# Kernel tuning notes

Measured on AMD Instinct MI355X. Metric: run time of the kernel, lower is better.

## Reference

```python
import jax, jax.numpy as jnp
import numpy as np

BN_EPS = 1e-5


def setup_inputs() -> dict:
    key = jax.random.key(0)
    ks = jax.random.split(key, 6)
    B, C, N = 8, 256, 2048
    C4 = C // 4
    return {
        "x": jax.random.normal(ks[0], (B, C, N), dtype=jnp.float32),
        "wq": jax.random.normal(ks[1], (C4, C), dtype=jnp.float32) * (1.0 / np.sqrt(C)),
        "wv": jax.random.normal(ks[2], (C, C), dtype=jnp.float32) * (1.0 / np.sqrt(C)),
        "bv": jax.random.normal(ks[3], (C,), dtype=jnp.float32) * 0.02,
        "wt": jax.random.normal(ks[4], (C, C), dtype=jnp.float32) * (1.0 / np.sqrt(C)),
        "bt": jax.random.normal(ks[5], (C,), dtype=jnp.float32) * 0.02,
        "gamma": jnp.ones((C,), dtype=jnp.float32),
        "beta": jnp.zeros((C,), dtype=jnp.float32),
    }


def reference(x, wq, wv, bv, wt, bt, gamma, beta):
    # x: [B, C, N]. Conv1d(kernel=1) == per-point matmul.
    # q_conv and k_conv share the same weight in the original, so q == k.
    q = jnp.einsum('oc,bcn->bon', wq, x)            # [B, C/4, N]
    # ||q_i - q_j||_2 via the Gram identity (same math as norm of the diff tensor)
    sq = jnp.sum(q * q, axis=1)                     # [B, N]
    gram = jnp.einsum('bci,bcj->bij', q, q)         # [B, N, N]
    d2 = sq[:, :, None] - 2.0 * gram + sq[:, None, :]
    l2 = jnp.sqrt(jnp.maximum(d2, 0.0))             # [B, N, N]
    attn = jax.nn.softmax(-l2, axis=-1)             # rows = queries i
    v = jnp.einsum('oc,bcn->bon', wv, x) + bv[None, :, None]   # [B, C, N]
    # einsum('bij,bkj->bik') then permute(0,2,1) == contract j directly to [B, C, N]
    x_r = jnp.einsum('bij,bcj->bci', attn, v)       # [B, C, N]
    t = jnp.einsum('oc,bcn->bon', wt, x_r) + bt[None, :, None]
    # BatchNorm1d in training mode: batch stats over (B, N), biased variance
    mean = jnp.mean(t, axis=(0, 2), keepdims=True)
    var = jnp.mean((t - mean) ** 2, axis=(0, 2), keepdims=True)
    bn = gamma[None, :, None] * (t - mean) * jax.lax.rsqrt(var + BN_EPS) + beta[None, :, None]
    return x + jnp.maximum(bn, 0.0)
```

## Files before the change

### kernel.cpp

```cpp
#include <hip/hip_runtime.h>
#include <math.h>

#define BDIM 8
#define CDIM 256
#define C4DIM 64
#define NDIM 2048
#define LOG2E_SQ 2.0813689810056077f
#define NEG_2LOG2E_SQ -4.1627379620112154f

typedef short bf16x8 __attribute__((ext_vector_type(8)));
typedef float f32x4 __attribute__((ext_vector_type(4)));

__device__ inline unsigned cvt_pk(float lo, float hi) {
  unsigned r;
  asm("v_cvt_pk_bf16_f32 %0, %1, %2" : "=v"(r) : "v"(lo), "v"(hi));
  return r;
}
__device__ inline float bflo(unsigned u) {
  u <<= 16; float f; __builtin_memcpy(&f, &u, 4); return f;
}
__device__ inline float bfhi(unsigned u) {
  u &= 0xffff0000u; float f; __builtin_memcpy(&f, &u, 4); return f;
}

__global__ __launch_bounds__(256) void castw_kernel(const float* __restrict__ wq,
                                                    const float* __restrict__ wv,
                                                    const float* __restrict__ wt,
                                                    short* __restrict__ wqb,
                                                    short* __restrict__ wvb,
                                                    short* __restrict__ wtb) {
  const int idx = (blockIdx.x * 256 + threadIdx.x) * 4;
  const float* src; short* dst; int off;
  if (idx < 16384)       { src = wq; dst = wqb; off = idx; }
  else if (idx < 81920)  { src = wv; dst = wvb; off = idx - 16384; }
  else                   { src = wt; dst = wtb; off = idx - 81920; }
  float4 v = *(const float4*)&src[off];
  uint2 u = make_uint2(cvt_pk(v.x, v.y), cvt_pk(v.z, v.w));
  *(uint2*)&dst[off] = u;
}

__global__ __launch_bounds__(256) void castT_kernel(const float* __restrict__ x,
                                                    short* __restrict__ xT) {
  __shared__ float tile[64][65];
  const int b = blockIdx.z, c0 = blockIdx.y * 64, n0 = blockIdx.x * 64;
  const int t = threadIdx.x;
  const int cl = t >> 2, ng = (t & 3) * 16;
#pragma unroll
  for (int kk = 0; kk < 4; ++kk) {
    float4 v = *(const float4*)&x[((size_t)(b * CDIM + c0 + cl)) * NDIM + n0 + ng + kk * 4];
    tile[cl][ng + kk * 4 + 0] = v.x; tile[cl][ng + kk * 4 + 1] = v.y;
    tile[cl][ng + kk * 4 + 2] = v.z; tile[cl][ng + kk * 4 + 3] = v.w;
  }
  __syncthreads();
  const int nl = t >> 2, cg = (t & 3) * 16;
  unsigned u[8];
#pragma unroll
  for (int e = 0; e < 8; ++e)
    u[e] = cvt_pk(tile[cg + 2 * e][nl], tile[cg + 2 * e + 1][nl]);
  short* dst = &xT[((size_t)b * NDIM + n0 + nl) * CDIM + c0 + cg];
  *(uint4*)&dst[0] = make_uint4(u[0], u[1], u[2], u[3]);
  *(uint4*)&dst[8] = make_uint4(u[4], u[5], u[6], u[7]);
}

__global__ __launch_bounds__(256) void qgemm_kernel(const short* __restrict__ wqb,
                                                    const short* __restrict__ xT,
                                                    short* __restrict__ qT,
                                                    float* __restrict__ sq2) {
  const int b = blockIdx.y, n0 = blockIdx.x * 64;
  const int t = threadIdx.x, w = t >> 6, l = t & 63, il = l & 15, g = l >> 4;
  const int nw = n0 + w * 16;
  f32x4 acc[4] = {};
#pragma unroll
  for (int ks = 0; ks < 8; ++ks) {
    const int k0 = ks * 32;
    bf16x8 bx = *(const bf16x8*)&xT[((size_t)b * NDIM + nw + il) * CDIM + k0 + g * 8];
#pragma unroll
    for (int ot = 0; ot < 4; ++ot) {
      bf16x8 aw = *(const bf16x8*)&wqb[(size_t)(ot * 16 + il) * CDIM + k0 + g * 8];
      acc[ot] = __builtin_amdgcn_mfma_f32_16x16x32_bf16(aw, bx, acc[ot], 0, 0, 0);
    }
  }
  float sqs = 0.f;
#pragma unroll
  for (int ot = 0; ot < 4; ++ot) {
    unsigned u0 = cvt_pk(acc[ot][0], acc[ot][1]);
    unsigned u1 = cvt_pk(acc[ot][2], acc[ot][3]);
    *(uint2*)&qT[((size_t)b * NDIM + nw + il) * C4DIM + ot * 16 + g * 4] = make_uint2(u0, u1);
    float f0 = bflo(u0), f1 = bfhi(u0), f2 = bflo(u1), f3 = bfhi(u1);
    sqs += f0 * f0 + f1 * f1 + f2 * f2 + f3 * f3;
  }
  sqs += __shfl_xor(sqs, 16, 64);
  sqs += __shfl_xor(sqs, 32, 64);
  if (l < 16) sq2[(size_t)b * NDIM + nw + l] = sqs * LOG2E_SQ;
}

template<bool F32OUT>
__global__ __launch_bounds__(256) void vt_gemm(const short* __restrict__ Wb,
                                               const short* __restrict__ Xt,
                                               const float* __restrict__ bias,
                                               void* __restrict__ OUTP,
                                               float* __restrict__ bnsum,
                                               float* __restrict__ bnss) {
  const int b = blockIdx.z, n0 = blockIdx.x * 128, c0 = blockIdx.y * 128;
  const int t = threadIdx.x, w = t >> 6, l = t & 63, il = l & 15, g = l >> 4;
  const int wn = w & 1, wc = w >> 1;
  const size_t arow = (size_t)b * NDIM + n0 + wn * 64;
  const int ccol = c0 + wc * 64;
  f32x4 acc[4][4] = {};
#pragma unroll
  for (int ks = 0; ks < 8; ++ks) {
    const int k0 = ks * 32;
    bf16x8 af[4], bf[4];
#pragma unroll
    for (int nt = 0; nt < 4; ++nt)
      af[nt] = *(const bf16x8*)&Xt[(arow + nt * 16 + il) * CDIM + k0 + g * 8];
#pragma unroll
    for (int ct = 0; ct < 4; ++ct)
      bf[ct] = *(const bf16x8*)&Wb[(size_t)(ccol + ct * 16 + il) * CDIM + k0 + g * 8];
#pragma unroll
    for (int nt = 0; nt < 4; ++nt)
#pragma unroll
      for (int ct = 0; ct < 4; ++ct)
        acc[nt][ct] = __builtin_amdgcn_mfma_f32_16x16x32_bf16(af[nt], bf[ct], acc[nt][ct], 0, 0, 0);
  }
#pragma unroll
  for (int ct = 0; ct < 4; ++ct) {
    const int c = ccol + ct * 16 + il;
    const float bs = bias[c];
    float s = 0.f, ss = 0.f;
#pragma unroll
    for (int nt = 0; nt < 4; ++nt) {
      const int n = n0 + wn * 64 + nt * 16 + g * 4;
      float y0 = acc[nt][ct][0] + bs, y1 = acc[nt][ct][1] + bs;
      float y2 = acc[nt][ct][2] + bs, y3 = acc[nt][ct][3] + bs;
      if (F32OUT) {
        *(float4*)&((float*)OUTP)[((size_t)(b * CDIM + c)) * NDIM + n] =
            make_float4(y0, y1, y2, y3);
        s += y0 + y1 + y2 + y3;
        ss += y0 * y0 + y1 * y1 + y2 * y2 + y3 * y3;
      } else {
        *(uint2*)&((short*)OUTP)[((size_t)(b * CDIM + c)) * NDIM + n] =
            make_uint2(cvt_pk(y0, y1), cvt_pk(y2, y3));
      }
    }
    if (F32OUT) {
      s += __shfl_xor(s, 16, 64);   s += __shfl_xor(s, 32, 64);
      ss += __shfl_xor(ss, 16, 64); ss += __shfl_xor(ss, 32, 64);
      if (l < 16) { atomicAdd(&bnsum[c], s); atomicAdd(&bnss[c], ss); }
    }
  }
}

__global__ __launch_bounds__(512) void attn_mfma(const short* __restrict__ qT,
                                                 const short* __restrict__ Vb16,
                                                 const float* __restrict__ sq2,
                                                 short* __restrict__ xrT) {
  __shared__ __align__(16) short vj[2][256 * 32];
  __shared__ __align__(16) short qj[2][32 * 64];
  __shared__ __align__(16) short wlds[4][16][40];
  __shared__ float sums[8][16];

  const int b  = blockIdx.y;
  const int i0 = blockIdx.x * 64;
  const int t  = threadIdx.x;
  const int w  = t >> 6, l = t & 63;
  const int il = l & 15, g = l >> 4;
  const int isub = w & 3, chalf = w >> 2;

  const short* qTb = qT + (size_t)b * NDIM * C4DIM;
  const short* Vbb = Vb16 + (size_t)b * CDIM * NDIM;
  const float* sqb = sq2 + (size_t)b * NDIM;

  const int iglob = i0 + isub * 16 + il;
  const bf16x8 bq0 = *(const bf16x8*)&qTb[(size_t)iglob * C4DIM + g * 8];
  const bf16x8 bq1 = *(const bf16x8*)&qTb[(size_t)iglob * C4DIM + 32 + g * 8];
  const float sqi = sqb[iglob];

  const int vc0 = t >> 2, vs0 = t & 3;
  const int vc1 = 128 + (t >> 2);
  const int vd0 = vc0 * 32 + ((vs0 ^ ((vc0 >> 1) & 3)) << 3);
  const int vd1 = vc1 * 32 + ((vs0 ^ ((vc1 >> 1) & 3)) << 3);
  const int qrow = t >> 3, qslot = t & 7;
  const int qd = qrow * 64 + ((qslot ^ (qrow & 7)) << 3);

  f32x4 acc[8];
#pragma unroll
  for (int k = 0; k < 8; ++k) acc[k] = {0.f, 0.f, 0.f, 0.f};
  float sumw = 0.f;

  f32x4 sqc;
  {
    bf16x8 vr0 = *(const bf16x8*)&Vbb[(size_t)vc0 * NDIM + vs0 * 8];
    bf16x8 vr1 = *(const bf16x8*)&Vbb[(size_t)vc1 * NDIM + vs0 * 8];
    *(bf16x8*)&vj[0][vd0] = vr0;
    *(bf16x8*)&vj[0][vd1] = vr1;
    if (w < 4) {
      bf16x8 qr = *(const bf16x8*)&qTb[(size_t)qrow * C4DIM + qslot * 8];
      *(bf16x8*)&qj[0][qd] = qr;
    }
    sqc = *(const f32x4*)&sqb[chalf * 16 + g * 4];
  }
  __syncthreads();

  const int NT = NDIM / 32;
  for (int jt = 0; jt < NT; ++jt) {
    const int p = jt & 1;
    const short* vbuf = &vj[p][0];
    const short* qbuf = &qj[p][0];
    short* vbufN = &vj[p ^ 1][0];
    short* qbufN = &qj[p ^ 1][0];
    const bool has_next = (jt + 1 < NT);
    const int j0n = jt * 32 + 32;

    bf16x8 vr0 = {}, vr1 = {}, qr = {};
    f32x4 sqn = {};
    if (has_next) {
      vr0 = *(const bf16x8*)&Vbb[(size_t)vc0 * NDIM + j0n + vs0 * 8];
      vr1 = *(const bf16x8*)&Vbb[(size_t)vc1 * NDIM + j0n + vs0 * 8];
      if (w < 4) qr = *(const bf16x8*)&qTb[(size_t)(j0n + qrow) * C4DIM + qslot * 8];
      sqn = *(const f32x4*)&sqb[j0n + chalf * 16 + g * 4];
    }

    {
      const int row = chalf * 16 + il;
      bf16x8 aJ0 = *(const bf16x8*)&qbuf[row * 64 + ((g ^ (il & 7)) << 3)];
      bf16x8 aJ1 = *(const bf16x8*)&qbuf[row * 64 + (((4 + g) ^ (il & 7)) << 3)];
      f32x4 s = {0.f, 0.f, 0.f, 0.f};
      s = __builtin_amdgcn_mfma_f32_16x16x32_bf16(aJ0, bq0, s, 0, 0, 0);
      s = __builtin_amdgcn_mfma_f32_16x16x32_bf16(aJ1, bq1, s, 0, 0, 0);
      float wv[4];
#pragma unroll
      for (int r = 0; r < 4; ++r) {
        float e = fmaxf(fmaf(NEG_2LOG2E_SQ, s[r], sqi + sqc[r]), 0.f);
        wv[r] = __builtin_amdgcn_exp2f(-__builtin_amdgcn_sqrtf(e));
        sumw += wv[r];
      }
      *(uint2*)&wlds[isub][il][chalf * 16 + g * 4] =
          make_uint2(cvt_pk(wv[0], wv[1]), cvt_pk(wv[2], wv[3]));
    }
    __syncthreads();

    const bf16x8 bw = *(const bf16x8*)&wlds[isub][il][g * 8];
#pragma unroll
    for (int ctl = 0; ctl < 8; ++ctl) {
      const int c = (chalf * 8 + ctl) * 16 + il;
      bf16x8 aV = *(const bf16x8*)&vbuf[c * 32 + ((g ^ ((il >> 1) & 3)) << 3)];
      acc[ctl] = __builtin_amdgcn_mfma_f32_16x16x32_bf16(aV, bw, acc[ctl], 0, 0, 0);
    }

    if (has_next) {
      *(bf16x8*)&vbufN[vd0] = vr0;
      *(bf16x8*)&vbufN[vd1] = vr1;
      if (w < 4) *(bf16x8*)&qbufN[qd] = qr;
      sqc = sqn;
    }
    __syncthreads();
  }

  sumw += __shfl_xor(sumw, 16, 64);
  sumw += __shfl_xor(sumw, 32, 64);
  if (l < 16) sums[w][l] = sumw;
  __syncthreads();
  const float inv = 1.f / (sums[w][il] + sums[w ^ 4][il]);
#pragma unroll
  for (int ctl = 0; ctl < 8; ++ctl) {
    float y0 = acc[ctl][0] * inv, y1 = acc[ctl][1] * inv;
    float y2 = acc[ctl][2] * inv, y3 = acc[ctl][3] * inv;
    *(uint2*)&xrT[((size_t)b * NDIM + iglob) * CDIM + (chalf * 8 + ctl) * 16 + g * 4] =
        make_uint2(cvt_pk(y0, y1), cvt_pk(y2, y3));
  }
}

__global__ __launch_bounds__(256) void bn_small(const float* __restrict__ bnsum,
                                                const float* __restrict__ bnss,
                                                const float* __restrict__ gamma,
                                                const float* __restrict__ beta,
                                                float* __restrict__ scale,
                                                float* __restrict__ shift) {
  const int c = threadIdx.x;
  const float cnt = (float)(BDIM * NDIM);
  const float mean = bnsum[c] / cnt;
  const float var = fmaxf(bnss[c] / cnt - mean * mean, 0.f);
  const float sc = gamma[c] * rsqrtf(var + 1e-5f);
  scale[c] = sc;
  shift[c] = beta[c] - mean * sc;
}

__global__ __launch_bounds__(256) void final_kernel(const float* __restrict__ x,
                                                    const float* __restrict__ scale,
                                                    const float* __restrict__ shift,
                                                    float* __restrict__ out) {
  const size_t idx = ((size_t)blockIdx.x * 256 + threadIdx.x) << 2;
  const int c = (int)((idx >> 11) & 255);
  float4 xv = *(const float4*)&x[idx];
  float4 tv = *(const float4*)&out[idx];
  const float sc = scale[c], sh = shift[c];
  float4 r;
  r.x = xv.x + fmaxf(tv.x * sc + sh, 0.f);
  r.y = xv.y + fmaxf(tv.y * sc + sh, 0.f);
  r.z = xv.z + fmaxf(tv.z * sc + sh, 0.f);
  r.w = xv.w + fmaxf(tv.w * sc + sh, 0.f);
  *(float4*)&out[idx] = r;
}

extern "C" void kernel_launch(void* const* d_in, const int* in_sizes, int n_in,
                              void* d_out, int out_size, void* d_ws, size_t ws_size,
                              hipStream_t stream) {
  const float* x     = (const float*)d_in[0];
  const float* wq    = (const float*)d_in[1];
  const float* wv    = (const float*)d_in[2];
  const float* bv    = (const float*)d_in[3];
  const float* wt    = (const float*)d_in[4];
  const float* bt    = (const float*)d_in[5];
  const float* gamma = (const float*)d_in[6];
  const float* beta  = (const float*)d_in[7];
  float* out = (float*)d_out;
  char* ws = (char*)d_ws;

  short* xbT   = (short*)(ws);
  short* wqb   = (short*)(ws + ((size_t)9  << 20));
  short* wvb   = (short*)(ws + ((size_t)9  << 20) + (256 << 10));
  short* wtb   = (short*)(ws + ((size_t)9  << 20) + (512 << 10));
  short* qT    = (short*)(ws + ((size_t)10 << 20));
  float* sq2   = (float*)(ws + ((size_t)12 << 20));
  short* vbf   = (short*)(ws + ((size_t)13 << 20));
  short* xrT   = (short*)(ws + ((size_t)22 << 20));
  float* bnsum = (float*)(ws + ((size_t)31 << 20));
  float* bnss  = bnsum + 256;
  float* scale = bnsum + 512;
  float* shift = bnsum + 768;

  castw_kernel<<<dim3(144), 256, 0, stream>>>(wq, wv, wt, wqb, wvb, wtb);
  castT_kernel<<<dim3(NDIM / 64, CDIM / 64, BDIM), 256, 0, stream>>>(x, xbT);
  qgemm_kernel<<<dim3(NDIM / 64, BDIM), 256, 0, stream>>>(wqb, xbT, qT, sq2);
  vt_gemm<false><<<dim3(NDIM / 128, CDIM / 128, BDIM), 256, 0, stream>>>(
      wvb, xbT, bv, vbf, nullptr, nullptr);
  attn_mfma<<<dim3(NDIM / 64, BDIM), 512, 0, stream>>>(qT, vbf, sq2, xrT);
  hipMemsetAsync((void*)bnsum, 0, 2048, stream);
  vt_gemm<true><<<dim3(NDIM / 128, CDIM / 128, BDIM), 256, 0, stream>>>(
      wtb, xrT, bt, out, bnsum, bnss);
  bn_small<<<dim3(1), 256, 0, stream>>>(bnsum, bnss, gamma, beta, scale, shift);
  final_kernel<<<dim3((BDIM * CDIM * NDIM) / (256 * 4)), 256, 0, stream>>>(x, scale, shift, out);
}
```

Measured before the change: 116.5 us.

## Merge launches, split attention over channel halves, store BN input as bf16

Combines the weight cast, input transpose-cast and BN-accumulator zeroing into one prep kernel. It also merges the q and v GEMMs into one launch and folds the BN scale/shift computation into the final kernel, cutting the launch count from nine to five. The attention kernel now uses 256-thread blocks, each handling one channel half with a swizzled block order. This removes one barrier per tile and the cross-wave sum exchange, but each block recomputes the distance weights for both halves. The pre-BN activations are written as bf16 instead of fp32, reducing traffic at the cost of precision in the batch-norm input.

```diff
diff --git a/kernel.cpp b/kernel.cpp
--- a/kernel.cpp
+++ b/kernel.cpp
@@ -23,86 +23,57 @@
   u &= 0xffff0000u; float f; __builtin_memcpy(&f, &u, 4); return f;
 }
 
-__global__ __launch_bounds__(256) void castw_kernel(const float* __restrict__ wq,
-                                                    const float* __restrict__ wv,
-                                                    const float* __restrict__ wt,
-                                                    short* __restrict__ wqb,
-                                                    short* __restrict__ wvb,
-                                                    short* __restrict__ wtb) {
-  const int idx = (blockIdx.x * 256 + threadIdx.x) * 4;
-  const float* src; short* dst; int off;
-  if (idx < 16384)       { src = wq; dst = wqb; off = idx; }
-  else if (idx < 81920)  { src = wv; dst = wvb; off = idx - 16384; }
-  else                   { src = wt; dst = wtb; off = idx - 81920; }
-  float4 v = *(const float4*)&src[off];
-  uint2 u = make_uint2(cvt_pk(v.x, v.y), cvt_pk(v.z, v.w));
-  *(uint2*)&dst[off] = u;
-}
-
-__global__ __launch_bounds__(256) void castT_kernel(const float* __restrict__ x,
-                                                    short* __restrict__ xT) {
+__global__ __launch_bounds__(256) void prep_kernel(const float* __restrict__ x,
+                                                   const float* __restrict__ wq,
+                                                   const float* __restrict__ wv,
+                                                   const float* __restrict__ wt,
+                                                   short* __restrict__ xT,
+                                                   short* __restrict__ wqb,
+                                                   short* __restrict__ wvb,
+                                                   short* __restrict__ wtb,
+                                                   float* __restrict__ bnsum) {
   __shared__ float tile[64][65];
-  const int b = blockIdx.z, c0 = blockIdx.y * 64, n0 = blockIdx.x * 64;
-  const int t = threadIdx.x;
-  const int cl = t >> 2, ng = (t & 3) * 16;
-#pragma unroll
-  for (int kk = 0; kk < 4; ++kk) {
-    float4 v = *(const float4*)&x[((size_t)(b * CDIM + c0 + cl)) * NDIM + n0 + ng + kk * 4];
-    tile[cl][ng + kk * 4 + 0] = v.x; tile[cl][ng + kk * 4 + 1] = v.y;
-    tile[cl][ng + kk * 4 + 2] = v.z; tile[cl][ng + kk * 4 + 3] = v.w;
-  }
-  __syncthreads();
-  const int nl = t >> 2, cg = (t & 3) * 16;
-  unsigned u[8];
-#pragma unroll
-  for (int e = 0; e < 8; ++e)
-    u[e] = cvt_pk(tile[cg + 2 * e][nl], tile[cg + 2 * e + 1][nl]);
-  short* dst = &xT[((size_t)b * NDIM + n0 + nl) * CDIM + c0 + cg];
-  *(uint4*)&dst[0] = make_uint4(u[0], u[1], u[2], u[3]);
-  *(uint4*)&dst[8] = make_uint4(u[4], u[5], u[6], u[7]);
-}
-
-__global__ __launch_bounds__(256) void qgemm_kernel(const short* __restrict__ wqb,
-                                                    const short* __restrict__ xT,
-                                                    short* __restrict__ qT,
-                                                    float* __restrict__ sq2) {
-  const int b = blockIdx.y, n0 = blockIdx.x * 64;
-  const int t = threadIdx.x, w = t >> 6, l = t & 63, il = l & 15, g = l >> 4;
-  const int nw = n0 + w * 16;
-  f32x4 acc[4] = {};
-#pragma unroll
-  for (int ks = 0; ks < 8; ++ks) {
-    const int k0 = ks * 32;
-    bf16x8 bx = *(const bf16x8*)&xT[((size_t)b * NDIM + nw + il) * CDIM + k0 + g * 8];
-#pragma unroll
-    for (int ot = 0; ot < 4; ++ot) {
-      bf16x8 aw = *(const bf16x8*)&wqb[(size_t)(ot * 16 + il) * CDIM + k0 + g * 8];
-      acc[ot] = __builtin_amdgcn_mfma_f32_16x16x32_bf16(aw, bx, acc[ot], 0, 0, 0);
-    }
-  }
-  float sqs = 0.f;
-#pragma unroll
-  for (int ot = 0; ot < 4; ++ot) {
-    unsigned u0 = cvt_pk(acc[ot][0], acc[ot][1]);
-    unsigned u1 = cvt_pk(acc[ot][2], acc[ot][3]);
-    *(uint2*)&qT[((size_t)b * NDIM + nw + il) * C4DIM + ot * 16 + g * 4] = make_uint2(u0, u1);
-    float f0 = bflo(u0), f1 = bfhi(u0), f2 = bflo(u1), f3 = bfhi(u1);
-    sqs += f0 * f0 + f1 * f1 + f2 * f2 + f3 * f3;
-  }
-  sqs += __shfl_xor(sqs, 16, 64);
-  sqs += __shfl_xor(sqs, 32, 64);
-  if (l < 16) sq2[(size_t)b * NDIM + nw + l] = sqs * LOG2E_SQ;
-}
-
-template<bool F32OUT>
-__global__ __launch_bounds__(256) void vt_gemm(const short* __restrict__ Wb,
-                                               const short* __restrict__ Xt,
-                                               const float* __restrict__ bias,
-                                               void* __restrict__ OUTP,
-                                               float* __restrict__ bnsum,
-                                               float* __restrict__ bnss) {
-  const int b = blockIdx.z, n0 = blockIdx.x * 128, c0 = blockIdx.y * 128;
-  const int t = threadIdx.x, w = t >> 6, l = t & 63, il = l & 15, g = l >> 4;
+  const int fb = blockIdx.x, t = threadIdx.x;
+  if (fb < 1024) {
+    const int b = fb >> 7, c0 = ((fb >> 5) & 3) * 64, n0 = (fb & 31) * 64;
+    const int cl = t >> 2, ng = (t & 3) * 16;
+#pragma unroll
+    for (int kk = 0; kk < 4; ++kk) {
+      float4 v = *(const float4*)&x[((size_t)(b * CDIM + c0 + cl)) * NDIM + n0 + ng + kk * 4];
+      tile[cl][ng + kk * 4 + 0] = v.x; tile[cl][ng + kk * 4 + 1] = v.y;
+      tile[cl][ng + kk * 4 + 2] = v.z; tile[cl][ng + kk * 4 + 3] = v.w;
+    }
+    __syncthreads();
+    const int nl = t >> 2, cg = (t & 3) * 16;
+    unsigned u[8];
+#pragma unroll
+    for (int e = 0; e < 8; ++e)
+      u[e] = cvt_pk(tile[cg + 2 * e][nl], tile[cg + 2 * e + 1][nl]);
+    short* dst = &xT[((size_t)b * NDIM + n0 + nl) * CDIM + c0 + cg];
+    *(uint4*)&dst[0] = make_uint4(u[0], u[1], u[2], u[3]);
+    *(uint4*)&dst[8] = make_uint4(u[4], u[5], u[6], u[7]);
+  } else if (fb < 1168) {
+    const int idx = ((fb - 1024) * 256 + t) * 4;
+    const float* src; short* dst; int off;
+    if (idx < 16384)      { src = wq; dst = wqb; off = idx; }
+    else if (idx < 81920) { src = wv; dst = wvb; off = idx - 16384; }
+    else                  { src = wt; dst = wtb; off = idx - 81920; }
+    float4 v = *(const float4*)&src[off];
+    *(uint2*)&dst[off] = make_uint2(cvt_pk(v.x, v.y), cvt_pk(v.z, v.w));
+  } else {
+    bnsum[t] = 0.f; bnsum[256 + t] = 0.f;
+  }
+}
+
+template<bool STATS>
+__device__ __forceinline__ void gemm128(const short* __restrict__ Wb,
+                                        const short* __restrict__ Xt,
+                                        const float* __restrict__ bias,
+                                        short* __restrict__ OUT,
+                                        float* __restrict__ bnsum,
+                                        float* __restrict__ bnss,
+                                        int b, int n0, int c0, int t) {
+  const int w = t >> 6, l = t & 63, il = l & 15, g = l >> 4;
   const int wn = w & 1, wc = w >> 1;
   const size_t arow = (size_t)b * NDIM + n0 + wn * 64;
   const int ccol = c0 + wc * 64;
@@ -110,18 +81,18 @@
 #pragma unroll
   for (int ks = 0; ks < 8; ++ks) {
     const int k0 = ks * 32;
-    bf16x8 af[4], bf[4];
+    bf16x8 af[4], bfr[4];
 #pragma unroll
     for (int nt = 0; nt < 4; ++nt)
       af[nt] = *(const bf16x8*)&Xt[(arow + nt * 16 + il) * CDIM + k0 + g * 8];
 #pragma unroll
     for (int ct = 0; ct < 4; ++ct)
-      bf[ct] = *(const bf16x8*)&Wb[(size_t)(ccol + ct * 16 + il) * CDIM + k0 + g * 8];
+      bfr[ct] = *(const bf16x8*)&Wb[(size_t)(ccol + ct * 16 + il) * CDIM + k0 + g * 8];
 #pragma unroll
     for (int nt = 0; nt < 4; ++nt)
 #pragma unroll
       for (int ct = 0; ct < 4; ++ct)
-        acc[nt][ct] = __builtin_amdgcn_mfma_f32_16x16x32_bf16(af[nt], bf[ct], acc[nt][ct], 0, 0, 0);
+        acc[nt][ct] = __builtin_amdgcn_mfma_f32_16x16x32_bf16(af[nt], bfr[ct], acc[nt][ct], 0, 0, 0);
   }
 #pragma unroll
   for (int ct = 0; ct < 4; ++ct) {
@@ -133,17 +104,14 @@
       const int n = n0 + wn * 64 + nt * 16 + g * 4;
       float y0 = acc[nt][ct][0] + bs, y1 = acc[nt][ct][1] + bs;
       float y2 = acc[nt][ct][2] + bs, y3 = acc[nt][ct][3] + bs;
-      if (F32OUT) {
-        *(float4*)&((float*)OUTP)[((size_t)(b * CDIM + c)) * NDIM + n] =
-            make_float4(y0, y1, y2, y3);
+      *(uint2*)&OUT[((size_t)(b * CDIM + c)) * NDIM + n] =
+          make_uint2(cvt_pk(y0, y1), cvt_pk(y2, y3));
+      if (STATS) {
         s += y0 + y1 + y2 + y3;
         ss += y0 * y0 + y1 * y1 + y2 * y2 + y3 * y3;
-      } else {
-        *(uint2*)&((short*)OUTP)[((size_t)(b * CDIM + c)) * NDIM + n] =
-            make_uint2(cvt_pk(y0, y1), cvt_pk(y2, y3));
       }
     }
-    if (F32OUT) {
+    if (STATS) {
       s += __shfl_xor(s, 16, 64);   s += __shfl_xor(s, 32, 64);
       ss += __shfl_xor(ss, 16, 64); ss += __shfl_xor(ss, 32, 64);
       if (l < 16) { atomicAdd(&bnsum[c], s); atomicAdd(&bnss[c], ss); }
@@ -151,35 +119,77 @@
   }
 }
 
-__global__ __launch_bounds__(512) void attn_mfma(const short* __restrict__ qT,
+__global__ __launch_bounds__(256) void qv_gemm(const short* __restrict__ wqb,
+                                               const short* __restrict__ wvb,
+                                               const short* __restrict__ xT,
+                                               const float* __restrict__ bv,
+                                               short* __restrict__ qT,
+                                               float* __restrict__ sq2,
+                                               short* __restrict__ vbf) {
+  const int fb = blockIdx.x, t = threadIdx.x;
+  if (fb < 256) {
+    const int b = fb >> 5, c0 = ((fb >> 4) & 1) * 128, n0 = (fb & 15) * 128;
+    gemm128<false>(wvb, xT, bv, vbf, nullptr, nullptr, b, n0, c0, t);
+  } else {
+    const int f = fb - 256;
+    const int b = f >> 5, n0 = (f & 31) * 64;
+    const int w = t >> 6, l = t & 63, il = l & 15, g = l >> 4;
+    const int nw = n0 + w * 16;
+    f32x4 acc[4] = {};
+#pragma unroll
+    for (int ks = 0; ks < 8; ++ks) {
+      const int k0 = ks * 32;
+      bf16x8 bx = *(const bf16x8*)&xT[((size_t)b * NDIM + nw + il) * CDIM + k0 + g * 8];
+#pragma unroll
+      for (int ot = 0; ot < 4; ++ot) {
+        bf16x8 aw = *(const bf16x8*)&wqb[(size_t)(ot * 16 + il) * CDIM + k0 + g * 8];
+        acc[ot] = __builtin_amdgcn_mfma_f32_16x16x32_bf16(aw, bx, acc[ot], 0, 0, 0);
+      }
+    }
+    float sqs = 0.f;
+#pragma unroll
+    for (int ot = 0; ot < 4; ++ot) {
+      unsigned u0 = cvt_pk(acc[ot][0], acc[ot][1]);
+      unsigned u1 = cvt_pk(acc[ot][2], acc[ot][3]);
+      *(uint2*)&qT[((size_t)b * NDIM + nw + il) * C4DIM + ot * 16 + g * 4] = make_uint2(u0, u1);
+      float f0 = bflo(u0), f1 = bfhi(u0), f2 = bflo(u1), f3 = bfhi(u1);
+      sqs += f0 * f0 + f1 * f1 + f2 * f2 + f3 * f3;
+    }
+    sqs += __shfl_xor(sqs, 16, 64);
+    sqs += __shfl_xor(sqs, 32, 64);
+    if (l < 16) sq2[(size_t)b * NDIM + nw + l] = sqs * LOG2E_SQ;
+  }
+}
+
+__global__ __launch_bounds__(256) void attn_mfma(const short* __restrict__ qT,
                                                  const short* __restrict__ Vb16,
                                                  const float* __restrict__ sq2,
                                                  short* __restrict__ xrT) {
-  __shared__ __align__(16) short vj[2][256 * 32];
+  __shared__ __align__(16) short vj[2][128 * 32];
   __shared__ __align__(16) short qj[2][32 * 64];
   __shared__ __align__(16) short wlds[4][16][40];
-  __shared__ float sums[8][16];
-
-  const int b  = blockIdx.y;
-  const int i0 = blockIdx.x * 64;
-  const int t  = threadIdx.x;
-  const int w  = t >> 6, l = t & 63;
-  const int il = l & 15, g = l >> 4;
-  const int isub = w & 3, chalf = w >> 2;
+
+  const int bid = blockIdx.x;
+  const int swz = (bid & 7) * 64 + (bid >> 3);
+  const int i0    = (swz & 31) * 64;
+  const int chalf = (swz >> 5) & 1;
+  const int b     = swz >> 6;
+
+  const int t = threadIdx.x;
+  const int w = t >> 6, l = t & 63, il = l & 15, g = l >> 4;
 
   const short* qTb = qT + (size_t)b * NDIM * C4DIM;
-  const short* Vbb = Vb16 + (size_t)b * CDIM * NDIM;
+  const short* Vbb = Vb16 + ((size_t)b * CDIM + chalf * 128) * NDIM;
   const float* sqb = sq2 + (size_t)b * NDIM;
 
-  const int iglob = i0 + isub * 16 + il;
+  const int iglob = i0 + w * 16 + il;
   const bf16x8 bq0 = *(const bf16x8*)&qTb[(size_t)iglob * C4DIM + g * 8];
   const bf16x8 bq1 = *(const bf16x8*)&qTb[(size_t)iglob * C4DIM + 32 + g * 8];
   const float sqi = sqb[iglob];
 
-  const int vc0 = t >> 2, vs0 = t & 3;
-  const int vc1 = 128 + (t >> 2);
-  const int vd0 = vc0 * 32 + ((vs0 ^ ((vc0 >> 1) & 3)) << 3);
-  const int vd1 = vc1 * 32 + ((vs0 ^ ((vc1 >> 1) & 3)) << 3);
+  const int vcb = t >> 2, vs = t & 3;
+  const int vd0 = vcb * 32 + ((vs ^ ((vcb >> 1) & 3)) << 3);
+  const int vd1 = vd0 + 64 * 32;
   const int qrow = t >> 3, qslot = t & 7;
   const int qd = qrow * 64 + ((qslot ^ (qrow & 7)) << 3);
 
@@ -188,17 +198,16 @@
   for (int k = 0; k < 8; ++k) acc[k] = {0.f, 0.f, 0.f, 0.f};
   float sumw = 0.f;
 
-  f32x4 sqc;
+  f32x4 sqc0, sqc1;
   {
-    bf16x8 vr0 = *(const bf16x8*)&Vbb[(size_t)vc0 * NDIM + vs0 * 8];
-    bf16x8 vr1 = *(const bf16x8*)&Vbb[(size_t)vc1 * NDIM + vs0 * 8];
+    bf16x8 vr0 = *(const bf16x8*)&Vbb[(size_t)vcb * NDIM + vs * 8];
+    bf16x8 vr1 = *(const bf16x8*)&Vbb[(size_t)(vcb + 64) * NDIM + vs * 8];
     *(bf16x8*)&vj[0][vd0] = vr0;
     *(bf16x8*)&vj[0][vd1] = vr1;
-    if (w < 4) {
-      bf16x8 qr = *(const bf16x8*)&qTb[(size_t)qrow * C4DIM + qslot * 8];
-      *(bf16x8*)&qj[0][qd] = qr;
-    }
-    sqc = *(const f32x4*)&sqb[chalf * 16 + g * 4];
+    bf16x8 qr = *(const bf16x8*)&qTb[(size_t)qrow * C4DIM + qslot * 8];
+    *(bf16x8*)&qj[0][qd] = qr;
+    sqc0 = *(const f32x4*)&sqb[g * 4];
+    sqc1 = *(const f32x4*)&sqb[16 + g * 4];
   }
   __syncthreads();
 
@@ -213,93 +222,97 @@
     const int j0n = jt * 32 + 32;
 
     bf16x8 vr0 = {}, vr1 = {}, qr = {};
-    f32x4 sqn = {};
+    f32x4 sqn0 = {}, sqn1 = {};
     if (has_next) {
-      vr0 = *(const bf16x8*)&Vbb[(size_t)vc0 * NDIM + j0n + vs0 * 8];
-      vr1 = *(const bf16x8*)&Vbb[(size_t)vc1 * NDIM + j0n + vs0 * 8];
-      if (w < 4) qr = *(const bf16x8*)&qTb[(size_t)(j0n + qrow) * C4DIM + qslot * 8];
-      sqn = *(const f32x4*)&sqb[j0n + chalf * 16 + g * 4];
-    }
-
-    {
-      const int row = chalf * 16 + il;
+      vr0 = *(const bf16x8*)&Vbb[(size_t)vcb * NDIM + j0n + vs * 8];
+      vr1 = *(const bf16x8*)&Vbb[(size_t)(vcb + 64) * NDIM + j0n + vs * 8];
+      qr  = *(const bf16x8*)&qTb[(size_t)(j0n + qrow) * C4DIM + qslot * 8];
+      sqn0 = *(const f32x4*)&sqb[j0n + g * 4];
+      sqn1 = *(const f32x4*)&sqb[j0n + 16 + g * 4];
+    }
+
+#pragma unroll
+    for (int h = 0; h < 2; ++h) {
+      const int row = h * 16 + il;
       bf16x8 aJ0 = *(const bf16x8*)&qbuf[row * 64 + ((g ^ (il & 7)) << 3)];
       bf16x8 aJ1 = *(const bf16x8*)&qbuf[row * 64 + (((4 + g) ^ (il & 7)) << 3)];
       f32x4 s = {0.f, 0.f, 0.f, 0.f};
       s = __builtin_amdgcn_mfma_f32_16x16x32_bf16(aJ0, bq0, s, 0, 0, 0);
       s = __builtin_amdgcn_mfma_f32_16x16x32_bf16(aJ1, bq1, s, 0, 0, 0);
+      const f32x4 sqh = h ? sqc1 : sqc0;
       float wv[4];
 #pragma unroll
       for (int r = 0; r < 4; ++r) {
-        float e = fmaxf(fmaf(NEG_2LOG2E_SQ, s[r], sqi + sqc[r]), 0.f);
+        float e = fmaxf(fmaf(NEG_2LOG2E_SQ, s[r], sqi + sqh[r]), 0.f);
         wv[r] = __builtin_amdgcn_exp2f(-__builtin_amdgcn_sqrtf(e));
         sumw += wv[r];
       }
-      *(uint2*)&wlds[isub][il][chalf * 16 + g * 4] =
+      *(uint2*)&wlds[w][il][h * 16 + g * 4] =
           make_uint2(cvt_pk(wv[0], wv[1]), cvt_pk(wv[2], wv[3]));
     }
-    __syncthreads();
-
-    const bf16x8 bw = *(const bf16x8*)&wlds[isub][il][g * 8];
+
+    const bf16x8 bw = *(const bf16x8*)&wlds[w][il][g * 8];
+
 #pragma unroll
     for (int ctl = 0; ctl < 8; ++ctl) {
-      const int c = (chalf * 8 + ctl) * 16 + il;
-      bf16x8 aV = *(const bf16x8*)&vbuf[c * 32 + ((g ^ ((il >> 1) & 3)) << 3)];
+      const int lr = ctl * 16 + il;
+      bf16x8 aV = *(const bf16x8*)&vbuf[lr * 32 + ((g ^ ((il >> 1) & 3)) << 3)];
       acc[ctl] = __builtin_amdgcn_mfma_f32_16x16x32_bf16(aV, bw, acc[ctl], 0, 0, 0);
     }
 
     if (has_next) {
       *(bf16x8*)&vbufN[vd0] = vr0;
       *(bf16x8*)&vbufN[vd1] = vr1;
-      if (w < 4) *(bf16x8*)&qbufN[qd] = qr;
-      sqc = sqn;
+      *(bf16x8*)&qbufN[qd] = qr;
+      sqc0 = sqn0; sqc1 = sqn1;
     }
     __syncthreads();
   }
 
   sumw += __shfl_xor(sumw, 16, 64);
   sumw += __shfl_xor(sumw, 32, 64);
-  if (l < 16) sums[w][l] = sumw;
-  __syncthreads();
-  const float inv = 1.f / (sums[w][il] + sums[w ^ 4][il]);
+  const float inv = 1.f / sumw;
 #pragma unroll
   for (int ctl = 0; ctl < 8; ++ctl) {
     float y0 = acc[ctl][0] * inv, y1 = acc[ctl][1] * inv;
     float y2 = acc[ctl][2] * inv, y3 = acc[ctl][3] * inv;
-    *(uint2*)&xrT[((size_t)b * NDIM + iglob) * CDIM + (chalf * 8 + ctl) * 16 + g * 4] =
+    *(uint2*)&xrT[((size_t)b * NDIM + iglob) * CDIM + chalf * 128 + ctl * 16 + g * 4] =
         make_uint2(cvt_pk(y0, y1), cvt_pk(y2, y3));
   }
 }
 
-__global__ __launch_bounds__(256) void bn_small(const float* __restrict__ bnsum,
-                                                const float* __restrict__ bnss,
-                                                const float* __restrict__ gamma,
-                                                const float* __restrict__ beta,
-                                                float* __restrict__ scale,
-                                                float* __restrict__ shift) {
-  const int c = threadIdx.x;
+__global__ __launch_bounds__(256) void t_gemm(const short* __restrict__ wtb,
+                                              const short* __restrict__ xrT,
+                                              const float* __restrict__ bt,
+                                              short* __restrict__ tbf,
+                                              float* __restrict__ bnsum,
+                                              float* __restrict__ bnss) {
+  gemm128<true>(wtb, xrT, bt, tbf, bnsum, bnss,
+                blockIdx.z, blockIdx.x * 128, blockIdx.y * 128, threadIdx.x);
+}
+
+__global__ __launch_bounds__(256) void final_kernel(const float* __restrict__ x,
+                                                    const short* __restrict__ tbf,
+                                                    const float* __restrict__ bnsum,
+                                                    const float* __restrict__ bnss,
+                                                    const float* __restrict__ gamma,
+                                                    const float* __restrict__ beta,
+                                                    float* __restrict__ out) {
+  const size_t idx = ((size_t)blockIdx.x * 256 + threadIdx.x) << 2;
+  const int c = (int)((idx >> 11) & 255);
   const float cnt = (float)(BDIM * NDIM);
   const float mean = bnsum[c] / cnt;
   const float var = fmaxf(bnss[c] / cnt - mean * mean, 0.f);
   const float sc = gamma[c] * rsqrtf(var + 1e-5f);
-  scale[c] = sc;
-  shift[c] = beta[c] - mean * sc;
-}
-
-__global__ __launch_bounds__(256) void final_kernel(const float* __restrict__ x,
-                                                    const float* __restrict__ scale,
-                                                    const float* __restrict__ shift,
-                                                    float* __restrict__ out) {
-  const size_t idx = ((size_t)blockIdx.x * 256 + threadIdx.x) << 2;
-  const int c = (int)((idx >> 11) & 255);
+  const float sh = beta[c] - mean * sc;
   float4 xv = *(const float4*)&x[idx];
-  float4 tv = *(const float4*)&out[idx];
-  const float sc = scale[c], sh = shift[c];
+  uint2 tu = *(const uint2*)&tbf[idx];
+  const float t0 = bflo(tu.x), t1 = bfhi(tu.x), t2 = bflo(tu.y), t3 = bfhi(tu.y);
   float4 r;
-  r.x = xv.x + fmaxf(tv.x * sc + sh, 0.f);
-  r.y = xv.y + fmaxf(tv.y * sc + sh, 0.f);
-  r.z = xv.z + fmaxf(tv.z * sc + sh, 0.f);
-  r.w = xv.w + fmaxf(tv.w * sc + sh, 0.f);
+  r.x = xv.x + fmaxf(t0 * sc + sh, 0.f);
+  r.y = xv.y + fmaxf(t1 * sc + sh, 0.f);
+  r.z = xv.z + fmaxf(t2 * sc + sh, 0.f);
+  r.w = xv.w + fmaxf(t3 * sc + sh, 0.f);
   *(float4*)&out[idx] = r;
 }
 
@@ -325,20 +338,13 @@
   float* sq2   = (float*)(ws + ((size_t)12 << 20));
   short* vbf   = (short*)(ws + ((size_t)13 << 20));
   short* xrT   = (short*)(ws + ((size_t)22 << 20));
+  short* tbf   = vbf;
   float* bnsum = (float*)(ws + ((size_t)31 << 20));
   float* bnss  = bnsum + 256;
-  float* scale = bnsum + 512;
-  float* shift = bnsum + 768;
-
-  castw_kernel<<<dim3(144), 256, 0, stream>>>(wq, wv, wt, wqb, wvb, wtb);
-  castT_kernel<<<dim3(NDIM / 64, CDIM / 64, BDIM), 256, 0, stream>>>(x, xbT);
-  qgemm_kernel<<<dim3(NDIM / 64, BDIM), 256, 0, stream>>>(wqb, xbT, qT, sq2);
-  vt_gemm<false><<<dim3(NDIM / 128, CDIM / 128, BDIM), 256, 0, stream>>>(
-      wvb, xbT, bv, vbf, nullptr, nullptr);
-  attn_mfma<<<dim3(NDIM / 64, BDIM), 512, 0, stream>>>(qT, vbf, sq2, xrT);
-  hipMemsetAsync((void*)bnsum, 0, 2048, stream);
-  vt_gemm<true><<<dim3(NDIM / 128, CDIM / 128, BDIM), 256, 0, stream>>>(
-      wtb, xrT, bt, out, bnsum, bnss);
-  bn_small<<<dim3(1), 256, 0, stream>>>(bnsum, bnss, gamma, beta, scale, shift);
-  final_kernel<<<dim3((BDIM * CDIM * NDIM) / (256 * 4)), 256, 0, stream>>>(x, scale, shift, out);
-}
+
+  prep_kernel<<<dim3(1169), 256, 0, stream>>>(x, wq, wv, wt, xbT, wqb, wvb, wtb, bnsum);
+  qv_gemm<<<dim3(512), 256, 0, stream>>>(wqb, wvb, xbT, bv, qT, sq2, vbf);
+  attn_mfma<<<dim3(512), 256, 0, stream>>>(qT, vbf, sq2, xrT);
+  t_gemm<<<dim3(16, 2, 8), 256, 0, stream>>>(wtb, xrT, bt, tbf, bnsum, bnss);
+  final_kernel<<<dim3(4096), 256, 0, stream>>>(x, tbf, bnsum, bnss, gamma, beta, out);
+}
```

New measurement: 103.3 us. 1.13x faster.
